# Performance work log

Measured on AMD Instinct MI355X. Metric: run time of the kernel, lower is better.

## Reference

```python
import jax, jax.numpy as jnp
import numpy as np

N, E, IN, H, D = 100000, 1600000, 128, 4, 64
NEG_SLOPE = 0.2
K_APPNP, ALPHA = 5, 0.5
BN_EPS = 1e-5


def setup_inputs() -> dict:
    key = jax.random.key(0)
    ks = jax.random.split(key, 12)
    return {
        'node_feats': jax.random.normal(ks[0], (N, IN), jnp.float32),
        'src': jax.random.randint(ks[1], (E,), 0, N, jnp.int32),
        'dst': jax.random.randint(ks[2], (E,), 0, N, jnp.int32),
        'W_fc': jax.random.normal(ks[3], (IN, H * D), jnp.float32) * (1.0 / np.sqrt(IN)),
        'attn_l': jax.random.normal(ks[4], (H, D), jnp.float32) * 0.1,
        'attn_r': jax.random.normal(ks[5], (H, D), jnp.float32) * 0.1,
        'W_res_gat': jax.random.normal(ks[6], (IN, H * D), jnp.float32) * (1.0 / np.sqrt(IN)),
        'gat_bias': jax.random.normal(ks[7], (H * D,), jnp.float32) * 0.01,
        'conv_w': jax.random.normal(ks[8], (1, H), jnp.float32) * 0.5,
        'conv_b': jax.random.normal(ks[9], (1,), jnp.float32) * 0.01,
        'W_res': jax.random.normal(ks[10], (D, IN), jnp.float32) * (1.0 / np.sqrt(IN)),
        'b_res': jax.random.normal(ks[11], (D,), jnp.float32) * 0.01,
        'gamma': jnp.ones((D,), jnp.float32),
        'beta': jnp.zeros((D,), jnp.float32),
    }


def reference(node_feats, src, dst, W_fc, attn_l, attn_r, W_res_gat, gat_bias,
              conv_w, conv_b, W_res, b_res, gamma, beta):
    # ---- GATConv (4 heads, residual, relu) ----
    feat = (node_feats @ W_fc).reshape(N, H, D)            # (N,H,D)
    el = jnp.einsum('nhd,hd->nh', feat, attn_l)            # (N,H)
    er = jnp.einsum('nhd,hd->nh', feat, attn_r)
    e = jax.nn.leaky_relu(el[src] + er[dst], NEG_SLOPE)    # (E,H)
    # edge softmax over incoming edges of each dst node
    emax = jax.ops.segment_max(e, dst, num_segments=N)     # (N,H)
    emax = jnp.where(jnp.isfinite(emax), emax, 0.0)
    ee = jnp.exp(e - emax[dst])                            # (E,H)
    denom = jax.ops.segment_sum(ee, dst, num_segments=N)   # (N,H)
    a = ee / jnp.maximum(denom[dst], 1e-9)                 # (E,H)
    msg = feat[src] * a[..., None]                         # (E,H,D)
    rst = jax.ops.segment_sum(msg, dst, num_segments=N)    # (N,H,D)
    resval = (node_feats @ W_res_gat).reshape(N, H, D)
    rst = jax.nn.relu(rst + resval + gat_bias.reshape(1, H, D))
    # ---- Conv1d (heads -> 1, kernel_size=1) then flatten ----
    h = jnp.einsum('nhd,oh->nod', rst, conv_w) + conv_b[None, :, None]
    h = h.reshape(N, D)
    # ---- APPNP (k=5, alpha=0.5), symmetric deg^{-1/2} norm (in-degree, clamp 1) ----
    deg = jax.ops.segment_sum(jnp.ones((E,), jnp.float32), dst, num_segments=N)
    norm = jnp.power(jnp.maximum(deg, 1.0), -0.5)[:, None]  # (N,1)
    h0 = h
    for _ in range(K_APPNP):
        h = jax.ops.segment_sum((h * norm)[src], dst, num_segments=N) * norm
        h = (1.0 - ALPHA) * h + ALPHA * h0
    # ---- residual linear + relu ----
    h = h + jax.nn.relu(node_feats @ W_res.T + b_res)
    # ---- BatchNorm1d (batch stats, affine) ----
    mu = h.mean(axis=0)
    var = h.var(axis=0)
    return (h - mu) * jax.lax.rsqrt(var + BN_EPS) * gamma + beta
```

## Files before the change

kernel.cpp:

```cpp
#include <hip/hip_runtime.h>
#include <math.h>

#define NN 100000
#define NE 1600000
#define NEG_SLOPE 0.2f
#define GB 98

typedef __attribute__((ext_vector_type(8))) short bf16x8;
typedef __attribute__((ext_vector_type(4))) float f32x4;
typedef __attribute__((ext_vector_type(2))) float f32x2;

__device__ __forceinline__ float b2f(unsigned short u) {
  union { unsigned u; float f; } c; c.u = ((unsigned)u) << 16; return c.f;
}
__device__ __forceinline__ unsigned short f2b(float x) {
  union { float f; unsigned u; } c; c.f = x;
  unsigned r = c.u + 0x7FFFu + ((c.u >> 16) & 1u);
  return (unsigned short)(r >> 16);
}
__device__ __forceinline__ void fma4(float4& acc, float s, const float4& b) {
  acc.x = fmaf(s, b.x, acc.x);
  acc.y = fmaf(s, b.y, acc.y);
  acc.z = fmaf(s, b.z, acc.z);
  acc.w = fmaf(s, b.w, acc.w);
}

__global__ __launch_bounds__(256) void k_zero(int* __restrict__ p, int nwords) {
  int i = blockIdx.x * 256 + threadIdx.x;
  if (i < nwords) p[i] = 0;
}

__global__ void k_zrow(unsigned short* __restrict__ a, unsigned short* __restrict__ b,
                       unsigned short* __restrict__ c) {
  int i = threadIdx.x;
  a[(size_t)NN * 64 + i] = 0;
  b[(size_t)NN * 64 + i] = 0;
  c[(size_t)NN * 64 + i] = 0;
}

__global__ __launch_bounds__(256) void k_cast(const float* __restrict__ A, unsigned short* __restrict__ Ab) {
  int i = blockIdx.x * 256 + threadIdx.x;
  int i4 = i * 4;
  if (i4 < NN * 128) {
    float4 v = *(const float4*)&A[i4];
    ushort4 o; o.x = f2b(v.x); o.y = f2b(v.y); o.z = f2b(v.z); o.w = f2b(v.w);
    *(ushort4*)&Ab[i4] = o;
  }
}

__global__ __launch_bounds__(256) void k_deg(const int* __restrict__ dst, int* __restrict__ deg) {
  int i = blockIdx.x * 256 + threadIdx.x;
  if (i < NE) atomicAdd(&deg[dst[i]], 1);
}

__global__ __launch_bounds__(256) void k_hist(const int* __restrict__ deg, int* __restrict__ bcount,
                                              int* __restrict__ bsum) {
  __shared__ int hist[64];
  __shared__ int red[256];
  int tid = threadIdx.x, blk = blockIdx.x;
  if (tid < 64) hist[tid] = 0;
  __syncthreads();
  int i0 = blk * 1024 + tid * 4;
  int s = 0;
#pragma unroll
  for (int r = 0; r < 4; ++r) {
    int i = i0 + r;
    if (i < NN) {
      int d = deg[i];
      s += d;
      atomicAdd(&hist[d < 63 ? d : 63], 1);
    }
  }
  red[tid] = s;
  __syncthreads();
  if (tid < 128) red[tid] += red[tid + 128];
  __syncthreads();
  if (tid < 64) {
    int v = red[tid] + red[tid + 64];
#pragma unroll
    for (int off = 32; off > 0; off >>= 1) v += __shfl_xor(v, off, 64);
    if (tid == 0) bsum[blk] = v;
    bcount[blk * 64 + tid] = hist[tid];
  }
}

__global__ void k_scan(int* __restrict__ bcount, const int* __restrict__ bsum,
                       int* __restrict__ dbase, int* __restrict__ bbase) {
  __shared__ int tot[64];
  int tid = threadIdx.x;
  {
    int s = 0;
#pragma unroll 7
    for (int blk = 0; blk < GB; ++blk) {
      int v = bcount[blk * 64 + tid];
      bcount[blk * 64 + tid] = s;
      s += v;
    }
    tot[tid] = s;
  }
  __syncthreads();
  if (tid == 0) {
    int base = 0;
    for (int b = 0; b < 64; ++b) { dbase[b] = base; base += tot[b]; }
  }
  if (tid == 1) {
    int s = 0;
#pragma unroll 7
    for (int blk = 0; blk < GB; ++blk) { bbase[blk] = s; s += bsum[blk]; }
  }
}

__global__ __launch_bounds__(256) void k_rows(const int* __restrict__ deg, const int* __restrict__ bcount,
                                              const int* __restrict__ dbase, const int* __restrict__ bbase,
                                              int* __restrict__ row_start, float* __restrict__ nrm,
                                              int* __restrict__ perm) {
  __shared__ int hist[64];
  __shared__ int sc[256];
  int tid = threadIdx.x, blk = blockIdx.x;
  if (tid < 64) hist[tid] = 0;
  int i0 = blk * 1024 + tid * 4;
  int d[4];
#pragma unroll
  for (int r = 0; r < 4; ++r) d[r] = (i0 + r < NN) ? deg[i0 + r] : 0;
  int ts = d[0] + d[1] + d[2] + d[3];
  sc[tid] = ts;
  __syncthreads();
  for (int off = 1; off < 256; off <<= 1) {
    int v = (tid >= off) ? sc[tid - off] : 0;
    __syncthreads();
    sc[tid] += v;
    __syncthreads();
  }
  int base = bbase[blk] + sc[tid] - ts;
#pragma unroll
  for (int r = 0; r < 4; ++r) {
    int i = i0 + r;
    if (i < NN) {
      row_start[i] = base;
      nrm[i] = rsqrtf(fmaxf((float)d[r], 1.0f));
      base += d[r];
      int b = d[r] < 63 ? d[r] : 63;
      int rank = atomicAdd(&hist[b], 1);
      perm[dbase[b] + bcount[blk * 64 + b] + rank] = i;
    }
  }
}

__global__ __launch_bounds__(256) void k_scatter(const int* __restrict__ src, const int* __restrict__ dst,
                                                 const int* __restrict__ row_start, int* __restrict__ cursor,
                                                 int* __restrict__ csr_src) {
  int i = blockIdx.x * 256 + threadIdx.x;
  if (i < NE) {
    int n = dst[i];
    int p = atomicAdd(&cursor[n], 1);
    csr_src[row_start[n] + p] = src[i];
  }
}

__global__ __launch_bounds__(256) void k_prepw(const float* __restrict__ W_fc, const float* __restrict__ al,
                                               const float* __restrict__ ar, float* __restrict__ w) {
  int o = blockIdx.x * 256 + threadIdx.x;
  if (o >= 1024) return;
  int side = o >> 9;
  int h = (o >> 7) & 3;
  int k = o & 127;
  const float* a = side ? ar : al;
  float s = 0.f;
  for (int d = 0; d < 64; ++d) s += W_fc[k * 256 + h * 64 + d] * a[h * 64 + d];
  w[(side * 4 + h) * 128 + k] = s;
}

__global__ __launch_bounds__(256) void k_elr2(const unsigned short* __restrict__ X, const float* __restrict__ w,
                                              float* __restrict__ el, float* __restrict__ er) {
  int n = blockIdx.x * 32 + (threadIdx.x >> 3);
  int p = threadIdx.x & 7;
  if (n >= NN) return;
  const uint4* xr = (const uint4*)(X + (size_t)n * 128);
  const float4* wr = (const float4*)(w + p * 128);
  float s = 0.f;
#pragma unroll
  for (int i = 0; i < 16; ++i) {
    uint4 x = xr[i];
    float4 w0 = wr[2 * i], w1 = wr[2 * i + 1];
    s += __uint_as_float(x.x << 16) * w0.x + __uint_as_float(x.x & 0xFFFF0000u) * w0.y
       + __uint_as_float(x.y << 16) * w0.z + __uint_as_float(x.y & 0xFFFF0000u) * w0.w
       + __uint_as_float(x.z << 16) * w1.x + __uint_as_float(x.z & 0xFFFF0000u) * w1.y
       + __uint_as_float(x.w << 16) * w1.z + __uint_as_float(x.w & 0xFFFF0000u) * w1.w;
  }
  if (p < 4) el[n * 4 + p] = s;
  else er[n * 4 + (p - 4)] = s;
}

__global__ __launch_bounds__(256) void k_prepB(const float* __restrict__ W_fc, const float* __restrict__ W_rg,
                                               unsigned short* __restrict__ Bp) {
  int y = blockIdx.y;
  const float* Bsrc = (y >> 1) ? W_rg : W_fc;
  int colbase = (y & 1) * 128;
  for (int e = blockIdx.x * 256 + threadIdx.x; e < 16384; e += 2048) {
    int n = e & 127, k = e >> 7;
    int p = colbase + n;
    int d = p >> 2, hh = p & 3;
    float v = Bsrc[k * 256 + hh * 64 + d];
    int nt = n >> 4, nn = n & 15, kt = k >> 5, quad = (k >> 3) & 3, j = k & 7;
    Bp[(size_t)y * 16384 + ((kt * 8 + nt) * 64 + quad * 16 + nn) * 8 + j] = f2b(v);
  }
}

__global__ __launch_bounds__(256) void k_gemm_mfma(const unsigned short* __restrict__ Abf,
                                                   const unsigned short* __restrict__ Bp,
                                                   unsigned* __restrict__ feat8u,
                                                   unsigned short* __restrict__ resval2) {
  __shared__ unsigned short Al[128 * 136];
  __shared__ unsigned short Bl[8192];
  int tid = threadIdx.x;
  int half = blockIdx.y >> 1;
  int colbase = (blockIdx.y & 1) * 128;
  int row0 = blockIdx.x * 128;
#pragma unroll
  for (int i = 0; i < 8; ++i) {
    int c = tid + i * 256;
    int row = c >> 4, part = c & 15;
    int gr = row0 + row; if (gr > NN - 1) gr = NN - 1;
    *(uint4*)&Al[row * 136 + part * 8] = *(const uint4*)&Abf[(size_t)gr * 128 + part * 8];
  }
  {
    const uint4* srcb = (const uint4*)(Bp + (size_t)blockIdx.y * 16384);
    uint4* dst4 = (uint4*)Bl;
#pragma unroll
    for (int i = 0; i < 4; ++i) dst4[tid + i * 256] = srcb[tid + i * 256];
  }
  __syncthreads();
  int w = tid >> 6, lane = tid & 63;
  int quad = lane >> 4, l16 = lane & 15;
  f32x4 acc[8][2];
#pragma unroll
  for (int rt = 0; rt < 8; ++rt)
#pragma unroll
    for (int c = 0; c < 2; ++c) acc[rt][c] = (f32x4){0.f, 0.f, 0.f, 0.f};
#pragma unroll
  for (int kh = 0; kh < 2; ++kh) {
    if (kh == 1) {
      __syncthreads();
      const uint4* srcb = (const uint4*)(Bp + (size_t)blockIdx.y * 16384 + 8192);
      uint4* dst4 = (uint4*)Bl;
#pragma unroll
      for (int i = 0; i < 4; ++i) dst4[tid + i * 256] = srcb[tid + i * 256];
      __syncthreads();
    }
#pragma unroll
    for (int ktl = 0; ktl < 2; ++ktl) {
      int kt = kh * 2 + ktl;
      bf16x8 b0 = *(const bf16x8*)&Bl[((ktl * 8 + w * 2 + 0) * 64 + lane) * 8];
      bf16x8 b1 = *(const bf16x8*)&Bl[((ktl * 8 + w * 2 + 1) * 64 + lane) * 8];
      int kb = kt * 32 + quad * 8;
#pragma unroll
      for (int rt = 0; rt < 8; ++rt) {
        bf16x8 a = *(const bf16x8*)&Al[(rt * 16 + l16) * 136 + kb];
        acc[rt][0] = __builtin_amdgcn_mfma_f32_16x16x32_bf16(b0, a, acc[rt][0], 0, 0, 0);
        acc[rt][1] = __builtin_amdgcn_mfma_f32_16x16x32_bf16(b1, a, acc[rt][1], 0, 0, 0);
      }
    }
  }
  __syncthreads();
  if (half == 0) {
    unsigned* Cl = (unsigned*)Al;
#pragma unroll
    for (int rt = 0; rt < 8; ++rt)
#pragma unroll
      for (int c = 0; c < 2; ++c) {
        int pk = __builtin_amdgcn_cvt_pk_fp8_f32(acc[rt][c][0], acc[rt][c][1], 0, false);
        pk = __builtin_amdgcn_cvt_pk_fp8_f32(acc[rt][c][2], acc[rt][c][3], pk, true);
        Cl[(rt * 16 + l16) * 36 + (w * 2 + c) * 4 + quad] = (unsigned)pk;
      }
    __syncthreads();
#pragma unroll
    for (int i = 0; i < 4; ++i) {
      int c = tid + i * 256;
      int row = c >> 3, wp = c & 7;
      int m = row0 + row;
      if (m < NN)
        *(uint4*)&feat8u[(size_t)m * 64 + (colbase >> 2) + wp * 4] = *(const uint4*)&Cl[row * 36 + wp * 4];
    }
  } else {
#pragma unroll
    for (int rt = 0; rt < 8; ++rt)
#pragma unroll
      for (int c = 0; c < 2; ++c) {
        int col = (w * 2 + c) * 16 + quad * 4;
        ushort4 o;
        o.x = f2b(acc[rt][c][0]); o.y = f2b(acc[rt][c][1]);
        o.z = f2b(acc[rt][c][2]); o.w = f2b(acc[rt][c][3]);
        *(ushort4*)&Al[(rt * 16 + l16) * 136 + col] = o;
      }
    __syncthreads();
#pragma unroll
    for (int i = 0; i < 8; ++i) {
      int c = tid + i * 256;
      int row = c >> 4, part = c & 15;
      int m = row0 + row;
      if (m < NN)
        *(uint4*)&resval2[(size_t)m * 256 + colbase + part * 8] = *(const uint4*)&Al[row * 136 + part * 8];
    }
  }
}

__global__ __launch_bounds__(256) void k_gemm_nt_bias_relu(const float* __restrict__ A, const float* __restrict__ B,
                                                           const float* __restrict__ bias, float* __restrict__ C) {
  __shared__ float Bl[128][68];
  for (int idx = threadIdx.x; idx < 64 * 128; idx += 256) {
    int d = idx >> 7, k = idx & 127;
    Bl[k][d] = B[d * 128 + k];
  }
  __syncthreads();
  int tx = threadIdx.x & 15, ty = threadIdx.x >> 4;
  int row0 = blockIdx.x * 64 + ty * 4;
  const float* ap[4];
#pragma unroll
  for (int r = 0; r < 4; ++r) ap[r] = A + (size_t)min(row0 + r, NN - 1) * 128;
  float4 acc[4];
#pragma unroll
  for (int r = 0; r < 4; ++r) acc[r] = make_float4(0.f, 0.f, 0.f, 0.f);
#pragma unroll 2
  for (int k0 = 0; k0 < 128; k0 += 4) {
    float4 b0 = *(const float4*)&Bl[k0][tx * 4];
    float4 b1 = *(const float4*)&Bl[k0 + 1][tx * 4];
    float4 b2 = *(const float4*)&Bl[k0 + 2][tx * 4];
    float4 b3 = *(const float4*)&Bl[k0 + 3][tx * 4];
#pragma unroll
    for (int r = 0; r < 4; ++r) {
      float4 a = *(const float4*)(ap[r] + k0);
      fma4(acc[r], a.x, b0); fma4(acc[r], a.y, b1);
      fma4(acc[r], a.z, b2); fma4(acc[r], a.w, b3);
    }
  }
  float4 bv = *(const float4*)&bias[tx * 4];
#pragma unroll
  for (int r = 0; r < 4; ++r) {
    int row = row0 + r;
    if (row < NN) {
      float4 v;
      v.x = fmaxf(acc[r].x + bv.x, 0.f);
      v.y = fmaxf(acc[r].y + bv.y, 0.f);
      v.z = fmaxf(acc[r].z + bv.z, 0.f);
      v.w = fmaxf(acc[r].w + bv.w, 0.f);
      *(float4*)&C[(size_t)row * 64 + tx * 4] = v;
    }
  }
}

__global__ __launch_bounds__(256) void k_gat(const int* __restrict__ perm, const int* __restrict__ row_start,
                                             const int* __restrict__ deg, const int* __restrict__ csr_src,
                                             const float* __restrict__ el, const float* __restrict__ er,
                                             const unsigned* __restrict__ feat8u,
                                             const unsigned short* __restrict__ resval2,
                                             const float* __restrict__ gat_bias, const float* __restrict__ conv_w,
                                             const float* __restrict__ conv_b, const float* __restrict__ nrm,
                                             float* __restrict__ h0, unsigned short* __restrict__ hs0o) {
  __shared__ int s_src[4][4][16];
  __shared__ float s_x[4][4][16][4];
  int wid = threadIdx.x >> 6, lane = threadIdx.x & 63;
  int g = lane >> 4, k = lane & 15;
  int n = perm[blockIdx.x * 16 + wid * 4 + g];
  int s0 = row_start[n], cnt = deg[n];
  float4 er4 = *(const float4*)&er[n * 4];
  unsigned koff = (unsigned)(k << 4);
  f32x2 a01[4], a23[4];
#pragma unroll
  for (int i = 0; i < 4; ++i) { a01[i] = (f32x2){0.f, 0.f}; a23[i] = (f32x2){0.f, 0.f}; }
  f32x2 den01 = (f32x2){0.f, 0.f}, den23 = (f32x2){0.f, 0.f};
  int cm = cnt;
  cm = max(cm, __shfl_xor(cm, 16, 64));
  cm = max(cm, __shfl_xor(cm, 32, 64));
  for (int base = 0; base < cm; base += 16) {
    int j = base + k;
    int s = 0;
    float x0 = 0.f, x1 = 0.f, x2 = 0.f, x3 = 0.f;
    if (j < cnt) {
      s = csr_src[s0 + j];
      float4 el4 = *(const float4*)&el[s * 4];
      float e0 = el4.x + er4.x; e0 = (e0 > 0.f) ? e0 : NEG_SLOPE * e0;
      float e1 = el4.y + er4.y; e1 = (e1 > 0.f) ? e1 : NEG_SLOPE * e1;
      float e2 = el4.z + er4.z; e2 = (e2 > 0.f) ? e2 : NEG_SLOPE * e2;
      float e3 = el4.w + er4.w; e3 = (e3 > 0.f) ? e3 : NEG_SLOPE * e3;
      x0 = __expf(e0); x1 = __expf(e1); x2 = __expf(e2); x3 = __expf(e3);
    }
    s_src[wid][g][k] = s;
    *(float4*)&s_x[wid][g][k][0] = make_float4(x0, x1, x2, x3);
    den01 += (f32x2){x0, x1}; den23 += (f32x2){x2, x3};
    int tm = cm - base; if (tm > 16) tm = 16;
    for (int t = 0; t < tm; ++t) {
      int s_ = s_src[wid][g][t];
      float4 x4 = *(const float4*)&s_x[wid][g][t][0];
      uint4 f = *(const uint4*)((const char*)feat8u + (((unsigned)s_ << 8) + koff));
      f32x2 x01 = (f32x2){x4.x, x4.y}, x23 = (f32x2){x4.z, x4.w};
      f32x2 lo, hi;
      lo = __builtin_amdgcn_cvt_pk_f32_fp8((int)f.x, false);
      hi = __builtin_amdgcn_cvt_pk_f32_fp8((int)f.x, true);
      a01[0] += x01 * lo; a23[0] += x23 * hi;
      lo = __builtin_amdgcn_cvt_pk_f32_fp8((int)f.y, false);
      hi = __builtin_amdgcn_cvt_pk_f32_fp8((int)f.y, true);
      a01[1] += x01 * lo; a23[1] += x23 * hi;
      lo = __builtin_amdgcn_cvt_pk_f32_fp8((int)f.z, false);
      hi = __builtin_amdgcn_cvt_pk_f32_fp8((int)f.z, true);
      a01[2] += x01 * lo; a23[2] += x23 * hi;
      lo = __builtin_amdgcn_cvt_pk_f32_fp8((int)f.w, false);
      hi = __builtin_amdgcn_cvt_pk_f32_fp8((int)f.w, true);
      a01[3] += x01 * lo; a23[3] += x23 * hi;
    }
  }
#pragma unroll
  for (int off = 1; off < 16; off <<= 1) {
    den01[0] += __shfl_xor(den01[0], off, 64);
    den01[1] += __shfl_xor(den01[1], off, 64);
    den23[0] += __shfl_xor(den23[0], off, 64);
    den23[1] += __shfl_xor(den23[1], off, 64);
  }
  float i0 = 1.f / fmaxf(den01[0], 1e-9f);
  float i1 = 1.f / fmaxf(den01[1], 1e-9f);
  float i2 = 1.f / fmaxf(den23[0], 1e-9f);
  float i3 = 1.f / fmaxf(den23[1], 1e-9f);
  uint4 rv0 = *(const uint4*)&resval2[(size_t)n * 256 + (k << 4)];
  uint4 rv1 = *(const uint4*)&resval2[(size_t)n * 256 + (k << 4) + 8];
  unsigned short c[16];
  *(uint4*)&c[0] = rv0; *(uint4*)&c[8] = rv1;
  int d0 = k << 2;
  float4 b0 = *(const float4*)&gat_bias[d0];
  float4 b1 = *(const float4*)&gat_bias[64 + d0];
  float4 b2 = *(const float4*)&gat_bias[128 + d0];
  float4 b3 = *(const float4*)&gat_bias[192 + d0];
  float bh0[4] = {b0.x, b0.y, b0.z, b0.w};
  float bh1[4] = {b1.x, b1.y, b1.z, b1.w};
  float bh2[4] = {b2.x, b2.y, b2.z, b2.w};
  float bh3[4] = {b3.x, b3.y, b3.z, b3.w};
  float cb = conv_b[0];
  float cw0 = conv_w[0], cw1 = conv_w[1], cw2 = conv_w[2], cw3 = conv_w[3];
  float hm[4];
#pragma unroll
  for (int i = 0; i < 4; ++i) {
    float t_, hmv = cb;
    t_ = fmaf(a01[i][0], i0, b2f(c[4 * i + 0]) + bh0[i]); t_ = fmaxf(t_, 0.f); hmv = fmaf(cw0, t_, hmv);
    t_ = fmaf(a01[i][1], i1, b2f(c[4 * i + 1]) + bh1[i]); t_ = fmaxf(t_, 0.f); hmv = fmaf(cw1, t_, hmv);
    t_ = fmaf(a23[i][0], i2, b2f(c[4 * i + 2]) + bh2[i]); t_ = fmaxf(t_, 0.f); hmv = fmaf(cw2, t_, hmv);
    t_ = fmaf(a23[i][1], i3, b2f(c[4 * i + 3]) + bh3[i]); t_ = fmaxf(t_, 0.f); hmv = fmaf(cw3, t_, hmv);
    hm[i] = hmv;
  }
  float nn_ = nrm[n];
  size_t o = (size_t)n * 64 + d0;
  *(float4*)&h0[o] = make_float4(hm[0], hm[1], hm[2], hm[3]);
  ushort4 hs;
  hs.x = f2b(hm[0] * nn_); hs.y = f2b(hm[1] * nn_);
  hs.z = f2b(hm[2] * nn_); hs.w = f2b(hm[3] * nn_);
  *(ushort4*)&hs0o[o] = hs;
}

__device__ __forceinline__ void gather4(const int* __restrict__ perm, const int* __restrict__ row_start,
                                        const int* __restrict__ deg, const int* __restrict__ csr_src,
                                        const unsigned short* __restrict__ hs_in,
                                        int wid, int lane, int& n, int& k, float (&a)[4]) {
  __shared__ int s_src[4][4][16];
  int g = lane >> 4; k = lane & 15;
  n = perm[blockIdx.x * 16 + wid * 4 + g];
  int s0 = row_start[n], cnt = deg[n];
  unsigned koff = (unsigned)(k << 3);
  a[0] = 0.f; a[1] = 0.f; a[2] = 0.f; a[3] = 0.f;
  int cm = cnt;
  cm = max(cm, __shfl_xor(cm, 16, 64));
  cm = max(cm, __shfl_xor(cm, 32, 64));
  for (int base = 0; base < cm; base += 16) {
    int j = base + k;
    s_src[wid][g][k] = (j < cnt) ? csr_src[s0 + j] : NN;
    int tm = cm - base; if (tm > 16) tm = 16;
    for (int t = 0; t < tm; ++t) {
      int s = s_src[wid][g][t];
      uint2 u = *(const uint2*)((const char*)hs_in + (((unsigned)s << 7) + koff));
      a[0] += __uint_as_float(u.x << 16);
      a[1] += __uint_as_float(u.x & 0xFFFF0000u);
      a[2] += __uint_as_float(u.y << 16);
      a[3] += __uint_as_float(u.y & 0xFFFF0000u);
    }
  }
}

__global__ __launch_bounds__(256) void k_gather_mid(const int* __restrict__ perm, const int* __restrict__ row_start,
                                                    const int* __restrict__ deg, const int* __restrict__ csr_src,
                                                    const unsigned short* __restrict__ hs_in,
                                                    const float* __restrict__ nrm,
                                                    const unsigned short* __restrict__ hs0,
                                                    unsigned short* __restrict__ hs_out) {
  int wid = threadIdx.x >> 6, lane = threadIdx.x & 63;
  int n, k; float a[4];
  gather4(perm, row_start, deg, csr_src, hs_in, wid, lane, n, k, a);
  size_t o = (size_t)n * 64 + (k << 2);
  float nn_ = nrm[n];
  float hnn = 0.5f * nn_ * nn_;
  uint2 z = *(const uint2*)&hs0[o];
  ushort4 ov;
  ov.x = f2b(fmaf(hnn, a[0], 0.5f * __uint_as_float(z.x << 16)));
  ov.y = f2b(fmaf(hnn, a[1], 0.5f * __uint_as_float(z.x & 0xFFFF0000u)));
  ov.z = f2b(fmaf(hnn, a[2], 0.5f * __uint_as_float(z.y << 16)));
  ov.w = f2b(fmaf(hnn, a[3], 0.5f * __uint_as_float(z.y & 0xFFFF0000u)));
  *(ushort4*)&hs_out[o] = ov;
}

__global__ __launch_bounds__(256) void k_gather_last(const int* __restrict__ perm, const int* __restrict__ row_start,
                                                     const int* __restrict__ deg, const int* __restrict__ csr_src,
                                                     const unsigned short* __restrict__ hs_in,
                                                     const float* __restrict__ nrm,
                                                     const float* __restrict__ res2,
                                                     float* h0io) {
  int wid = threadIdx.x >> 6, lane = threadIdx.x & 63;
  int n, k; float a[4];
  gather4(perm, row_start, deg, csr_src, hs_in, wid, lane, n, k, a);
  size_t o = (size_t)n * 64 + (k << 2);
  float nn_ = nrm[n];
  float hn = 0.5f * nn_;
  float4 h4 = *(const float4*)&h0io[o];
  float4 r4 = *(const float4*)&res2[o];
  float4 v;
  v.x = fmaf(hn, a[0], 0.5f * h4.x) + r4.x;
  v.y = fmaf(hn, a[1], 0.5f * h4.y) + r4.y;
  v.z = fmaf(hn, a[2], 0.5f * h4.z) + r4.z;
  v.w = fmaf(hn, a[3], 0.5f * h4.w) + r4.w;
  *(float4*)&h0io[o] = v;
}

__global__ __launch_bounds__(256) void k_finred(const float* __restrict__ hfin, float* __restrict__ bn) {
  __shared__ float s1[256], s2[256];
  int d = threadIdx.x & 63;
  int rb = blockIdx.x * 64;
  float sum = 0.f, sq = 0.f;
  for (int r = threadIdx.x >> 6; r < 64; r += 4) {
    int n = rb + r;
    if (n < NN) {
      float v = hfin[(size_t)n * 64 + d];
      sum += v; sq += v * v;
    }
  }
  s1[threadIdx.x] = sum; s2[threadIdx.x] = sq;
  __syncthreads();
  if (threadIdx.x < 128) { s1[threadIdx.x] += s1[threadIdx.x + 128]; s2[threadIdx.x] += s2[threadIdx.x + 128]; }
  __syncthreads();
  if (threadIdx.x < 64) {
    atomicAdd(&bn[d], s1[threadIdx.x] + s1[threadIdx.x + 64]);
    atomicAdd(&bn[64 + d], s2[threadIdx.x] + s2[threadIdx.x + 64]);
  }
}

__global__ void k_bnstats(const float* __restrict__ bn, const float* __restrict__ gamma,
                          const float* __restrict__ beta, float* __restrict__ bns) {
  int d = threadIdx.x;
  float mu = bn[d] * (1.0f / NN);
  float var = fmaxf(bn[64 + d] * (1.0f / NN) - mu * mu, 0.f);
  float sc = rsqrtf(var + 1e-5f) * gamma[d];
  bns[d] = sc;
  bns[64 + d] = beta[d] - mu * sc;
}

__global__ __launch_bounds__(256) void k_bnapply(const float* __restrict__ h, const float* __restrict__ bns,
                                                 float* __restrict__ out) {
  int i = blockIdx.x * 256 + threadIdx.x;
  if (i < NN * 64) {
    int d = i & 63;
    out[i] = fmaf(h[i], bns[d], bns[64 + d]);
  }
}

extern "C" void kernel_launch(void* const* d_in, const int* in_sizes, int n_in,
                              void* d_out, int out_size, void* d_ws, size_t ws_size,
                              hipStream_t stream) {
  const float* node_feats = (const float*)d_in[0];
  const int* src = (const int*)d_in[1];
  const int* dst = (const int*)d_in[2];
  const float* W_fc = (const float*)d_in[3];
  const float* attn_l = (const float*)d_in[4];
  const float* attn_r = (const float*)d_in[5];
  const float* W_res_gat = (const float*)d_in[6];
  const float* gat_bias = (const float*)d_in[7];
  const float* conv_w = (const float*)d_in[8];
  const float* conv_b = (const float*)d_in[9];
  const float* W_res = (const float*)d_in[10];
  const float* b_res = (const float*)d_in[11];
  const float* gamma = (const float*)d_in[12];
  const float* beta = (const float*)d_in[13];
  float* out = (float*)d_out;

  char* base = (char*)d_ws;
  size_t off = 0;
  auto alloc = [&](size_t bytes) -> char* {
    char* p = base + off;
    off = (off + bytes + 255) & ~(size_t)255;
    return p;
  };
  unsigned* feat8u        = (unsigned*)alloc((size_t)NN * 256);
  unsigned short* resval2 = (unsigned short*)alloc((size_t)NN * 256 * 2);
  float* res2             = (float*)resval2;
  float* el               = (float*)alloc((size_t)NN * 4 * 4);
  float* er               = (float*)alloc((size_t)NN * 4 * 4);
  float* h0               = (float*)alloc((size_t)NN * 64 * 4);
  unsigned short* Abf     = (unsigned short*)h0;
  unsigned short* hs0     = (unsigned short*)alloc((size_t)(NN + 1) * 64 * 2);
  unsigned short* hsA     = (unsigned short*)alloc((size_t)(NN + 1) * 64 * 2);
  unsigned short* hsB     = (unsigned short*)alloc((size_t)(NN + 1) * 64 * 2);
  int* csr_src            = (int*)alloc((size_t)NE * 4);
  float* nrm              = (float*)alloc((size_t)NN * 4);
  int* row_start          = (int*)alloc((size_t)NN * 4);
  int* perm               = (int*)alloc((size_t)NN * 4);
  int* bcount             = (int*)alloc((size_t)GB * 64 * 4);
  int* bsum               = (int*)alloc((size_t)GB * 4);
  int* bbase              = (int*)alloc((size_t)GB * 4);
  int* dbase              = (int*)alloc(64 * 4);
  unsigned short* Bpacked = (unsigned short*)alloc((size_t)4 * 16384 * 2);
  float* w_elr            = (float*)alloc((size_t)8 * 128 * 4);
  size_t zoff = off;
  int* deg                = (int*)alloc((size_t)NN * 4);
  int* cursor             = (int*)alloc((size_t)NN * 4);
  float* bn               = (float*)alloc(256 * 4);
  float* hfin             = h0;

  int zwords = (int)((off - zoff) / 4);
  int gE = (NE + 255) / 256;
  int gP = NN / 16;
  int gM = (NN + 63) / 64;
  int gV = (NN * 64 + 255) / 256;

  k_zero<<<(zwords + 255) / 256, 256, 0, stream>>>((int*)(base + zoff), zwords);
  k_zrow<<<1, 64, 0, stream>>>(hs0, hsA, hsB);
  k_deg<<<gE, 256, 0, stream>>>(dst, deg);
  k_hist<<<GB, 256, 0, stream>>>(deg, bcount, bsum);
  k_scan<<<1, 64, 0, stream>>>(bcount, bsum, dbase, bbase);
  k_rows<<<GB, 256, 0, stream>>>(deg, bcount, dbase, bbase, row_start, nrm, perm);
  k_scatter<<<gE, 256, 0, stream>>>(src, dst, row_start, cursor, csr_src);

  k_cast<<<(NN * 128 / 4 + 255) / 256, 256, 0, stream>>>(node_feats, Abf);
  k_prepB<<<dim3(8, 4), 256, 0, stream>>>(W_fc, W_res_gat, Bpacked);
  k_prepw<<<4, 256, 0, stream>>>(W_fc, attn_l, attn_r, w_elr);
  k_gemm_mfma<<<dim3((NN + 127) / 128, 4), 256, 0, stream>>>(Abf, Bpacked, feat8u, resval2);

  k_elr2<<<(NN + 31) / 32, 256, 0, stream>>>(Abf, w_elr, el, er);
  k_gat<<<gP, 256, 0, stream>>>(perm, row_start, deg, csr_src, el, er, feat8u, resval2,
                                gat_bias, conv_w, conv_b, nrm, h0, hs0);

  k_gemm_nt_bias_relu<<<gM, 256, 0, stream>>>(node_feats, W_res, b_res, res2);

  k_gather_mid<<<gP, 256, 0, stream>>>(perm, row_start, deg, csr_src, hs0, nrm, hs0, hsA);
  k_gather_mid<<<gP, 256, 0, stream>>>(perm, row_start, deg, csr_src, hsA, nrm, hs0, hsB);
  k_gather_mid<<<gP, 256, 0, stream>>>(perm, row_start, deg, csr_src, hsB, nrm, hs0, hsA);
  k_gather_mid<<<gP, 256, 0, stream>>>(perm, row_start, deg, csr_src, hsA, nrm, hs0, hsB);
  k_gather_last<<<gP, 256, 0, stream>>>(perm, row_start, deg, csr_src, hsB, nrm, res2, hfin);

  k_finred<<<gM, 256, 0, stream>>>(hfin, bn);
  k_bnstats<<<1, 64, 0, stream>>>(bn, gamma, beta, bn + 128);
  k_bnapply<<<gV, 256, 0, stream>>>(hfin, bn + 128, out);
}
```

Before: 734.3 us.

## Scramble block-to-node-chunk mapping and unroll gather loops with transposed LDS indices

Blocks now pick their 16-node chunk through a multiplicative hash of the block index, so degree-sorted chunks are spread across CUs instead of heavy nodes clustering in time. The edge loops in the GAT and APPNP gather kernels are unrolled by 2 and 4 to issue several independent global loads per iteration, and the shared-memory index arrays are transposed. This aims to balance the load and expose more memory-level parallelism. Padded iterations rely on sentinel sources (a zero row at NN, or zero weights in GAT), which adds extra loads for odd counts.

```diff
diff --git a/kernel.cpp b/kernel.cpp
--- a/kernel.cpp
+++ b/kernel.cpp
@@ -5,6 +5,8 @@
 #define NE 1600000
 #define NEG_SLOPE 0.2f
 #define GB 98
+#define GP 6250
+#define SCR 2411u
 
 typedef __attribute__((ext_vector_type(8))) short bf16x8;
 typedef __attribute__((ext_vector_type(4))) float f32x4;
@@ -356,11 +358,12 @@
                                              const float* __restrict__ gat_bias, const float* __restrict__ conv_w,
                                              const float* __restrict__ conv_b, const float* __restrict__ nrm,
                                              float* __restrict__ h0, unsigned short* __restrict__ hs0o) {
-  __shared__ int s_src[4][4][16];
-  __shared__ float s_x[4][4][16][4];
+  __shared__ int s_src[4][16][4];
+  __shared__ float s_x[4][16][4][4];
   int wid = threadIdx.x >> 6, lane = threadIdx.x & 63;
   int g = lane >> 4, k = lane & 15;
-  int n = perm[blockIdx.x * 16 + wid * 4 + g];
+  int chunk = (int)(((unsigned)blockIdx.x * SCR) % (unsigned)GP);
+  int n = perm[chunk * 16 + wid * 4 + g];
   int s0 = row_start[n], cnt = deg[n];
   float4 er4 = *(const float4*)&er[n * 4];
   unsigned koff = (unsigned)(k << 4);
@@ -383,29 +386,51 @@
       float e2 = el4.z + er4.z; e2 = (e2 > 0.f) ? e2 : NEG_SLOPE * e2;
       float e3 = el4.w + er4.w; e3 = (e3 > 0.f) ? e3 : NEG_SLOPE * e3;
       x0 = __expf(e0); x1 = __expf(e1); x2 = __expf(e2); x3 = __expf(e3);
-    }
-    s_src[wid][g][k] = s;
-    *(float4*)&s_x[wid][g][k][0] = make_float4(x0, x1, x2, x3);
-    den01 += (f32x2){x0, x1}; den23 += (f32x2){x2, x3};
+      den01 += (f32x2){x0, x1}; den23 += (f32x2){x2, x3};
+    }
+    s_src[wid][k][g] = s;
+    *(float4*)&s_x[wid][k][g][0] = make_float4(x0, x1, x2, x3);
     int tm = cm - base; if (tm > 16) tm = 16;
-    for (int t = 0; t < tm; ++t) {
-      int s_ = s_src[wid][g][t];
-      float4 x4 = *(const float4*)&s_x[wid][g][t][0];
-      uint4 f = *(const uint4*)((const char*)feat8u + (((unsigned)s_ << 8) + koff));
-      f32x2 x01 = (f32x2){x4.x, x4.y}, x23 = (f32x2){x4.z, x4.w};
-      f32x2 lo, hi;
-      lo = __builtin_amdgcn_cvt_pk_f32_fp8((int)f.x, false);
-      hi = __builtin_amdgcn_cvt_pk_f32_fp8((int)f.x, true);
-      a01[0] += x01 * lo; a23[0] += x23 * hi;
-      lo = __builtin_amdgcn_cvt_pk_f32_fp8((int)f.y, false);
-      hi = __builtin_amdgcn_cvt_pk_f32_fp8((int)f.y, true);
-      a01[1] += x01 * lo; a23[1] += x23 * hi;
-      lo = __builtin_amdgcn_cvt_pk_f32_fp8((int)f.z, false);
-      hi = __builtin_amdgcn_cvt_pk_f32_fp8((int)f.z, true);
-      a01[2] += x01 * lo; a23[2] += x23 * hi;
-      lo = __builtin_amdgcn_cvt_pk_f32_fp8((int)f.w, false);
-      hi = __builtin_amdgcn_cvt_pk_f32_fp8((int)f.w, true);
-      a01[3] += x01 * lo; a23[3] += x23 * hi;
+    int tm2 = (tm + 1) & ~1;
+    for (int t = 0; t < tm2; t += 2) {
+      int sa = s_src[wid][t][g];
+      int sb = s_src[wid][t + 1][g];
+      uint4 fa = *(const uint4*)((const char*)feat8u + (((unsigned)sa << 8) + koff));
+      uint4 fb = *(const uint4*)((const char*)feat8u + (((unsigned)sb << 8) + koff));
+      float4 xa = *(const float4*)&s_x[wid][t][g][0];
+      float4 xb = *(const float4*)&s_x[wid][t + 1][g][0];
+      {
+        f32x2 x01 = (f32x2){xa.x, xa.y}, x23 = (f32x2){xa.z, xa.w};
+        f32x2 lo, hi;
+        lo = __builtin_amdgcn_cvt_pk_f32_fp8((int)fa.x, false);
+        hi = __builtin_amdgcn_cvt_pk_f32_fp8((int)fa.x, true);
+        a01[0] += x01 * lo; a23[0] += x23 * hi;
+        lo = __builtin_amdgcn_cvt_pk_f32_fp8((int)fa.y, false);
+        hi = __builtin_amdgcn_cvt_pk_f32_fp8((int)fa.y, true);
+        a01[1] += x01 * lo; a23[1] += x23 * hi;
+        lo = __builtin_amdgcn_cvt_pk_f32_fp8((int)fa.z, false);
+        hi = __builtin_amdgcn_cvt_pk_f32_fp8((int)fa.z, true);
+        a01[2] += x01 * lo; a23[2] += x23 * hi;
+        lo = __builtin_amdgcn_cvt_pk_f32_fp8((int)fa.w, false);
+        hi = __builtin_amdgcn_cvt_pk_f32_fp8((int)fa.w, true);
+        a01[3] += x01 * lo; a23[3] += x23 * hi;
+      }
+      {
+        f32x2 x01 = (f32x2){xb.x, xb.y}, x23 = (f32x2){xb.z, xb.w};
+        f32x2 lo, hi;
+        lo = __builtin_amdgcn_cvt_pk_f32_fp8((int)fb.x, false);
+        hi = __builtin_amdgcn_cvt_pk_f32_fp8((int)fb.x, true);
+        a01[0] += x01 * lo; a23[0] += x23 * hi;
+        lo = __builtin_amdgcn_cvt_pk_f32_fp8((int)fb.y, false);
+        hi = __builtin_amdgcn_cvt_pk_f32_fp8((int)fb.y, true);
+        a01[1] += x01 * lo; a23[1] += x23 * hi;
+        lo = __builtin_amdgcn_cvt_pk_f32_fp8((int)fb.z, false);
+        hi = __builtin_amdgcn_cvt_pk_f32_fp8((int)fb.z, true);
+        a01[2] += x01 * lo; a23[2] += x23 * hi;
+        lo = __builtin_amdgcn_cvt_pk_f32_fp8((int)fb.w, false);
+        hi = __builtin_amdgcn_cvt_pk_f32_fp8((int)fb.w, true);
+        a01[3] += x01 * lo; a23[3] += x23 * hi;
+      }
     }
   }
 #pragma unroll
@@ -457,9 +482,10 @@
                                         const int* __restrict__ deg, const int* __restrict__ csr_src,
                                         const unsigned short* __restrict__ hs_in,
                                         int wid, int lane, int& n, int& k, float (&a)[4]) {
-  __shared__ int s_src[4][4][16];
+  __shared__ int s_src[4][16][4];
   int g = lane >> 4; k = lane & 15;
-  n = perm[blockIdx.x * 16 + wid * 4 + g];
+  int chunk = (int)(((unsigned)blockIdx.x * SCR) % (unsigned)GP);
+  n = perm[chunk * 16 + wid * 4 + g];
   int s0 = row_start[n], cnt = deg[n];
   unsigned koff = (unsigned)(k << 3);
   a[0] = 0.f; a[1] = 0.f; a[2] = 0.f; a[3] = 0.f;
@@ -468,15 +494,26 @@
   cm = max(cm, __shfl_xor(cm, 32, 64));
   for (int base = 0; base < cm; base += 16) {
     int j = base + k;
-    s_src[wid][g][k] = (j < cnt) ? csr_src[s0 + j] : NN;
+    s_src[wid][k][g] = (j < cnt) ? csr_src[s0 + j] : NN;
     int tm = cm - base; if (tm > 16) tm = 16;
-    for (int t = 0; t < tm; ++t) {
-      int s = s_src[wid][g][t];
-      uint2 u = *(const uint2*)((const char*)hs_in + (((unsigned)s << 7) + koff));
-      a[0] += __uint_as_float(u.x << 16);
-      a[1] += __uint_as_float(u.x & 0xFFFF0000u);
-      a[2] += __uint_as_float(u.y << 16);
-      a[3] += __uint_as_float(u.y & 0xFFFF0000u);
+    int tm4 = (tm + 3) & ~3;
+    for (int t = 0; t < tm4; t += 4) {
+      int sa = s_src[wid][t][g];
+      int sb = s_src[wid][t + 1][g];
+      int sc2 = s_src[wid][t + 2][g];
+      int sd = s_src[wid][t + 3][g];
+      uint2 ua = *(const uint2*)((const char*)hs_in + (((unsigned)sa << 7) + koff));
+      uint2 ub = *(const uint2*)((const char*)hs_in + (((unsigned)sb << 7) + koff));
+      uint2 uc = *(const uint2*)((const char*)hs_in + (((unsigned)sc2 << 7) + koff));
+      uint2 ud = *(const uint2*)((const char*)hs_in + (((unsigned)sd << 7) + koff));
+      a[0] += __uint_as_float(ua.x << 16) + __uint_as_float(ub.x << 16);
+      a[1] += __uint_as_float(ua.x & 0xFFFF0000u) + __uint_as_float(ub.x & 0xFFFF0000u);
+      a[2] += __uint_as_float(ua.y << 16) + __uint_as_float(ub.y << 16);
+      a[3] += __uint_as_float(ua.y & 0xFFFF0000u) + __uint_as_float(ub.y & 0xFFFF0000u);
+      a[0] += __uint_as_float(uc.x << 16) + __uint_as_float(ud.x << 16);
+      a[1] += __uint_as_float(uc.x & 0xFFFF0000u) + __uint_as_float(ud.x & 0xFFFF0000u);
+      a[2] += __uint_as_float(uc.y << 16) + __uint_as_float(ud.y << 16);
+      a[3] += __uint_as_float(uc.y & 0xFFFF0000u) + __uint_as_float(ud.y & 0xFFFF0000u);
     }
   }
 }
@@ -619,7 +656,6 @@
 
   int zwords = (int)((off - zoff) / 4);
   int gE = (NE + 255) / 256;
-  int gP = NN / 16;
   int gM = (NN + 63) / 64;
   int gV = (NN * 64 + 255) / 256;
 
@@ -637,16 +673,16 @@
   k_gemm_mfma<<<dim3((NN + 127) / 128, 4), 256, 0, stream>>>(Abf, Bpacked, feat8u, resval2);
 
   k_elr2<<<(NN + 31) / 32, 256, 0, stream>>>(Abf, w_elr, el, er);
-  k_gat<<<gP, 256, 0, stream>>>(perm, row_start, deg, csr_src, el, er, feat8u, resval2,
+  k_gat<<<GP, 256, 0, stream>>>(perm, row_start, deg, csr_src, el, er, feat8u, resval2,
                                 gat_bias, conv_w, conv_b, nrm, h0, hs0);
 
   k_gemm_nt_bias_relu<<<gM, 256, 0, stream>>>(node_feats, W_res, b_res, res2);
 
-  k_gather_mid<<<gP, 256, 0, stream>>>(perm, row_start, deg, csr_src, hs0, nrm, hs0, hsA);
-  k_gather_mid<<<gP, 256, 0, stream>>>(perm, row_start, deg, csr_src, hsA, nrm, hs0, hsB);
-  k_gather_mid<<<gP, 256, 0, stream>>>(perm, row_start, deg, csr_src, hsB, nrm, hs0, hsA);
-  k_gather_mid<<<gP, 256, 0, stream>>>(perm, row_start, deg, csr_src, hsA, nrm, hs0, hsB);
-  k_gather_last<<<gP, 256, 0, stream>>>(perm, row_start, deg, csr_src, hsB, nrm, res2, hfin);
+  k_gather_mid<<<GP, 256, 0, stream>>>(perm, row_start, deg, csr_src, hs0, nrm, hs0, hsA);
+  k_gather_mid<<<GP, 256, 0, stream>>>(perm, row_start, deg, csr_src, hsA, nrm, hs0, hsB);
+  k_gather_mid<<<GP, 256, 0, stream>>>(perm, row_start, deg, csr_src, hsB, nrm, hs0, hsA);
+  k_gather_mid<<<GP, 256, 0, stream>>>(perm, row_start, deg, csr_src, hsA, nrm, hs0, hsB);
+  k_gather_last<<<GP, 256, 0, stream>>>(perm, row_start, deg, csr_src, hsB, nrm, res2, hfin);
 
   k_finred<<<gM, 256, 0, stream>>>(hfin, bn);
   k_bnstats<<<1, 64, 0, stream>>>(bn, gamma, beta, bn + 128);
```

New measurement: 729.0 us (median of 2 runs). About the same (-0.7%).
